# Kernel tuning notes

Measured on AMD Instinct MI355X. Metric: run time of the kernel, lower is better.

Reference implementation:

```python
import jax, jax.numpy as jnp
import numpy as np

N, IN_DIM, H, ATT_DIM, OUT_DIM = 4096, 512, 8, 64, 64
ATT_BIAS = 0.5


def setup_inputs() -> dict:
    key = jax.random.key(0)
    ks = jax.random.split(key, 12)
    s_in = 1.0 / np.sqrt(IN_DIM)
    s_o = 1.0 / np.sqrt(H * OUT_DIM)
    return {
        "Q": jax.random.normal(ks[0], (N, IN_DIM), jnp.float32),
        "K": jax.random.normal(ks[1], (N, IN_DIM), jnp.float32),
        "V": jax.random.normal(ks[2], (N, IN_DIM), jnp.float32),
        "adj": jax.random.uniform(ks[3], (N, N), jnp.float32),
        "WQ": jax.random.normal(ks[4], (IN_DIM, H * ATT_DIM), jnp.float32) * s_in,
        "bQ": jnp.zeros((H * ATT_DIM,), jnp.float32),
        "WK": jax.random.normal(ks[5], (IN_DIM, H * ATT_DIM), jnp.float32) * s_in,
        "bK": jnp.zeros((H * ATT_DIM,), jnp.float32),
        "WV": jax.random.normal(ks[6], (IN_DIM, H * OUT_DIM), jnp.float32) * s_in,
        "bV": jnp.zeros((H * OUT_DIM,), jnp.float32),
        "WO": jax.random.normal(ks[7], (H * OUT_DIM, OUT_DIM), jnp.float32) * s_o,
        "bO": jnp.zeros((OUT_DIM,), jnp.float32),
    }


def reference(Q, K, V, adj, WQ, bQ, WK, bK, WV, bV, WO, bO):
    scale = ATT_DIM ** -0.5
    q = (Q @ WQ + bQ).reshape(N, H, ATT_DIM)   # [N,H,d]
    k = (K @ WK + bK).reshape(N, H, ATT_DIM)   # [N,H,d]
    v = (V @ WV + bV).reshape(N, H, OUT_DIM)   # [N,H,e]
    # scaled QK^T per head: [H,N,N]
    scores = jnp.einsum("nhd,mhd->hnm", q * scale, k)
    # sigmoid -> bias subtract -> +0.1*adj -> softmax over keys
    scores = jax.nn.sigmoid(scores) - ATT_BIAS + 0.1 * adj[None, :, :]
    attn = jax.nn.softmax(scores, axis=2)
    # attend values (dropout p=0 => identity), concat heads, project
    out = jnp.einsum("hnm,mhe->nhe", attn, v).reshape(N, H * OUT_DIM)
    return out @ WO + bO
```

## Files before the change

kernel.cpp:

```cpp
#include <hip/hip_runtime.h>
#include <hip/hip_bf16.h>

#define N_TOK  4096
#define HD     512
#define NH     8
#define NSPLIT 4

typedef short v8s __attribute__((ext_vector_type(8)));
typedef float v4f __attribute__((ext_vector_type(4)));
typedef unsigned short u16;

#if __has_builtin(__builtin_amdgcn_exp2f)
#define USE_EXP2 1
#define ADJ_SCALE 0.14426950408889634f
#else
#define USE_EXP2 0
#define ADJ_SCALE 0.1f
#endif

__device__ __forceinline__ float bf2f(u16 x) {
  union { unsigned int u; float f; } c; c.u = ((unsigned int)x) << 16; return c.f;
}
__device__ __forceinline__ u16 f2bf(float f) {
  union { float f; unsigned int u; } c; c.f = f;
  return (u16)((c.u + 0x7fffu + ((c.u >> 16) & 1u)) >> 16);
}

__global__ void detect_k(const u16* __restrict__ q, int* __restrict__ flag) {
  int l = threadIdx.x;
  u16 e = q[2 * l];
  float x = bf2f(e);
  int ex = (e >> 7) & 0xFF;
  float ax = fabsf(x);
  bool ok = (ex != 0xFF) && (ax < 64.f) && (ax > 1e-30f);
  unsigned long long m = __ballot(ok);
  if (l == 0) *flag = (__popcll(m) >= 48) ? 0 : 1;
}

__global__ __launch_bounds__(256) void conv_qkv_k(const void* __restrict__ s0, const void* __restrict__ s1,
                                                  const void* __restrict__ s2,
                                                  u16* __restrict__ d0, u16* __restrict__ d1,
                                                  u16* __restrict__ d2, const int* __restrict__ flag) {
  int z = blockIdx.y;
  const void* s = (z == 0) ? s0 : (z == 1) ? s1 : s2;
  u16* d = (z == 0) ? d0 : (z == 1) ? d1 : d2;
  int i = blockIdx.x * 256 + threadIdx.x;
  short4 o;
  if (*flag) {
    float4 f = ((const float4*)s)[i];
    o.x = (short)f2bf(f.x); o.y = (short)f2bf(f.y);
    o.z = (short)f2bf(f.z); o.w = (short)f2bf(f.w);
  } else {
    o = ((const short4*)s)[i];
  }
  ((short4*)d)[i] = o;
}

__global__ __launch_bounds__(256) void conv_adj_k(const void* __restrict__ src, u16* __restrict__ dst,
                                                  const int* __restrict__ flag) {
  int i = blockIdx.x * 256 + threadIdx.x;
  float4 f;
  if (*flag) {
    f = ((const float4*)src)[i];
  } else {
    short4 v = ((const short4*)src)[i];
    f.x = bf2f((u16)v.x); f.y = bf2f((u16)v.y); f.z = bf2f((u16)v.z); f.w = bf2f((u16)v.w);
  }
  short4 o;
  o.x = (short)f2bf(f.x * ADJ_SCALE); o.y = (short)f2bf(f.y * ADJ_SCALE);
  o.z = (short)f2bf(f.z * ADJ_SCALE); o.w = (short)f2bf(f.w * ADJ_SCALE);
  ((short4*)dst)[i] = o;
}

__global__ void conv_bias_k(const void* sQ, const void* sK, const void* sV, const void* sO,
                            u16* dQ, u16* dK, u16* dV, u16* dO, const int* __restrict__ flag) {
  int i = blockIdx.x * 256 + threadIdx.x;
  const void* s; u16* d; int off;
  if (i < 512)       { s = sQ; d = dQ; off = i; }
  else if (i < 1024) { s = sK; d = dK; off = i - 512; }
  else if (i < 1536) { s = sV; d = dV; off = i - 1024; }
  else if (i < 1600) { s = sO; d = dO; off = i - 1536; }
  else return;
  float v = (*flag) ? ((const float*)s)[off] : bf2f(((const u16*)s)[off]);
  d[off] = f2bf(v);
}

__global__ __launch_bounds__(256) void tr_w_k(const void* W0, const void* W1, const void* W2, const void* W3,
                                              u16* t0, u16* t1, u16* t2, u16* t3,
                                              const int* __restrict__ flag) {
  int z = blockIdx.z;
  const void* in; u16* out; int C;
  if (z == 0)      { in = W0; out = t0; C = 512; }
  else if (z == 1) { in = W1; out = t1; C = 512; }
  else if (z == 2) { in = W2; out = t2; C = 512; }
  else             { in = W3; out = t3; C = 64; if (blockIdx.y) return; }
  const int R = 512;
  __shared__ __align__(16) u16 tile[64][72];
  const int r0 = blockIdx.x * 64, c0 = blockIdx.y * 64;
  const int t = threadIdx.x;
  bool f32 = (*flag) != 0;
#pragma unroll
  for (int rep = 0; rep < 2; ++rep) {
    int idx = (t + rep * 256) * 8;
    int r = idx >> 6, c = idx & 63;
    if (f32) {
      const float* sp = (const float*)in + (size_t)(r0 + r) * C + (c0 + c);
      float4 a = *(const float4*)sp, b = *(const float4*)(sp + 4);
      u16 tmp[8] = { f2bf(a.x), f2bf(a.y), f2bf(a.z), f2bf(a.w),
                     f2bf(b.x), f2bf(b.y), f2bf(b.z), f2bf(b.w) };
      *(v8s*)&tile[r][c] = *(v8s*)tmp;
    } else {
      *(v8s*)&tile[r][c] = *(const v8s*)((const u16*)in + (size_t)(r0 + r) * C + (c0 + c));
    }
  }
  __syncthreads();
#pragma unroll
  for (int rep = 0; rep < 2; ++rep) {
    int idx = (t + rep * 256) * 8;
    int oc = idx >> 6, orr = idx & 63;
    u16 tmp[8];
#pragma unroll
    for (int j = 0; j < 8; ++j) tmp[j] = tile[orr + j][oc];
    *(v8s*)(out + (size_t)(c0 + oc) * R + (r0 + orr)) = *(v8s*)tmp;
  }
}

__global__ __launch_bounds__(256) void tr_bf16(const u16* __restrict__ in, u16* __restrict__ out,
                                               int R, int C) {
  __shared__ __align__(16) u16 tile[64][72];
  const int r0 = blockIdx.x * 64, c0 = blockIdx.y * 64;
  const int t = threadIdx.x;
#pragma unroll
  for (int rep = 0; rep < 2; ++rep) {
    int idx = (t + rep * 256) * 8;
    int r = idx >> 6, c = idx & 63;
    *(v8s*)&tile[r][c] = *(const v8s*)(in + (size_t)(r0 + r) * C + (c0 + c));
  }
  __syncthreads();
#pragma unroll
  for (int rep = 0; rep < 2; ++rep) {
    int idx = (t + rep * 256) * 8;
    int oc = idx >> 6, orr = idx & 63;
    u16 tmp[8];
#pragma unroll
    for (int j = 0; j < 8; ++j) tmp[j] = tile[orr + j][oc];
    *(v8s*)(out + (size_t)(c0 + oc) * R + (r0 + orr)) = *(v8s*)tmp;
  }
}

__device__ __forceinline__ void gemm_body(const u16* __restrict__ A, const u16* __restrict__ Bt,
                                          const u16* __restrict__ bias, void* __restrict__ C,
                                          bool f32o, int NB, int K) {
  __shared__ __align__(16) u16 As[64][72];
  __shared__ __align__(16) u16 Bs[64][72];
  const int i0 = blockIdx.x * 64, j0 = blockIdx.y * 64;
  const int t = threadIdx.x, w = t >> 6, l = t & 63, quad = l >> 4, l15 = l & 15;
  v4f acc[4] = {};
  for (int k0 = 0; k0 < K; k0 += 64) {
#pragma unroll
    for (int rep = 0; rep < 2; ++rep) {
      int idx = (t + rep * 256) * 8;
      int r = idx >> 6, c = idx & 63;
      *(v8s*)&As[r][c] = *(const v8s*)(A + (size_t)(i0 + r) * K + k0 + c);
      *(v8s*)&Bs[r][c] = *(const v8s*)(Bt + (size_t)(j0 + r) * K + k0 + c);
    }
    __syncthreads();
#pragma unroll
    for (int h = 0; h < 2; ++h) {
      v8s a = *(const v8s*)&As[w * 16 + l15][h * 32 + quad * 8];
#pragma unroll
      for (int cb = 0; cb < 4; ++cb) {
        v8s b = *(const v8s*)&Bs[cb * 16 + l15][h * 32 + quad * 8];
        acc[cb] = __builtin_amdgcn_mfma_f32_16x16x32_bf16(a, b, acc[cb], 0, 0, 0);
      }
    }
    __syncthreads();
  }
#pragma unroll
  for (int cb = 0; cb < 4; ++cb) {
    int col = j0 + cb * 16 + l15;
    float bv = bf2f(bias[col]);
#pragma unroll
    for (int r = 0; r < 4; ++r) {
      int row = blockIdx.x * 64 + w * 16 + quad * 4 + r;
      float v = acc[cb][r] + bv;
      size_t idx = (size_t)row * NB + col;
      if (f32o) ((float*)C)[idx] = v;
      else      ((u16*)C)[idx] = f2bf(v);
    }
  }
}

__global__ __launch_bounds__(256) void gemm_qkv_k(const u16* __restrict__ Ac0, const u16* __restrict__ Ac1,
                                                  const u16* __restrict__ Ac2,
                                                  const u16* __restrict__ t0, const u16* __restrict__ t1,
                                                  const u16* __restrict__ t2,
                                                  const u16* __restrict__ b0, const u16* __restrict__ b1,
                                                  const u16* __restrict__ b2,
                                                  u16* __restrict__ o0, u16* __restrict__ o1,
                                                  u16* __restrict__ o2) {
  int z = blockIdx.z;
  const u16* A  = (z == 0) ? Ac0 : (z == 1) ? Ac1 : Ac2;
  const u16* Bt = (z == 0) ? t0  : (z == 1) ? t1  : t2;
  const u16* bi = (z == 0) ? b0  : (z == 1) ? b1  : b2;
  u16* C        = (z == 0) ? o0  : (z == 1) ? o1  : o2;
  gemm_body(A, Bt, bi, C, false, HD, 512);
}

__global__ __launch_bounds__(256) void gemm_bt(const u16* __restrict__ A, const u16* __restrict__ Bt,
                                               const u16* __restrict__ bias, void* __restrict__ C,
                                               const int* __restrict__ outflag, int NB, int K) {
  gemm_body(A, Bt, bias, C, (*outflag) != 0, NB, K);
}

__global__ __launch_bounds__(256) void attn_kernel(const u16* __restrict__ qb, const u16* __restrict__ kb,
                                                   const u16* __restrict__ vtb, const u16* __restrict__ adjc,
                                                   u16* __restrict__ Opart, float* __restrict__ Lpart) {
  __shared__ __align__(16) u16 Ks[64][72];
  __shared__ __align__(16) u16 Vs[64][72];
  __shared__ __align__(16) u16 Adjs[64][72];
  __shared__ __align__(16) u16 Ps[4][16][72];
  const int i0 = blockIdx.x * 64;
  const int h64 = blockIdx.y * 64;
  const int z = blockIdx.z;
  const int m_begin = z * (N_TOK / NSPLIT);
  const int m_end = m_begin + (N_TOK / NSPLIT);
  const int t = threadIdx.x, w = t >> 6, l = t & 63, quad = l >> 4, l15 = l & 15;

  v8s qf[2];
#pragma unroll
  for (int h = 0; h < 2; ++h)
    qf[h] = *(const v8s*)(qb + (size_t)(i0 + w * 16 + l15) * HD + h64 + h * 32 + quad * 8);

  v4f oacc[4] = {};
  float lsum[4] = {0.f, 0.f, 0.f, 0.f};

  for (int m0 = m_begin; m0 < m_end; m0 += 64) {
#pragma unroll
    for (int rep = 0; rep < 2; ++rep) {
      int idx = (t + rep * 256) * 8;
      int r = idx >> 6, c = idx & 63;
      *(v8s*)&Ks[r][c]   = *(const v8s*)(kb   + (size_t)(m0 + r) * HD + h64 + c);
      *(v8s*)&Vs[r][c]   = *(const v8s*)(vtb  + (size_t)(h64 + r) * N_TOK + m0 + c);
      *(v8s*)&Adjs[r][c] = *(const v8s*)(adjc + (size_t)(i0 + r) * N_TOK + m0 + c);
    }
    __syncthreads();

    v4f s[4] = {};
#pragma unroll
    for (int h = 0; h < 2; ++h) {
#pragma unroll
      for (int cb = 0; cb < 4; ++cb) {
        v8s b = *(const v8s*)&Ks[cb * 16 + l15][h * 32 + quad * 8];
        s[cb] = __builtin_amdgcn_mfma_f32_16x16x32_bf16(qf[h], b, s[cb], 0, 0, 0);
      }
    }

#pragma unroll
    for (int cb = 0; cb < 4; ++cb) {
#pragma unroll
      for (int r = 0; r < 4; ++r) {
        float sraw = s[cb][r];
        float d = bf2f(Adjs[w * 16 + quad * 4 + r][cb * 16 + l15]);
#if USE_EXP2
        float u = __builtin_amdgcn_exp2f(sraw * -0.18033688f);
        float sig = __builtin_amdgcn_rcpf(1.f + u);
        float p = __builtin_amdgcn_exp2f(fmaf(sig, 1.44269504f, d - 0.72134752f));
#else
        float u = __expf(sraw * -0.125f);
        float sig = __builtin_amdgcn_rcpf(1.f + u);
        float p = __expf(sig + (d - 0.5f));
#endif
        lsum[r] += p;
        Ps[w][quad * 4 + r][cb * 16 + l15] = f2bf(p);
      }
    }
    asm volatile("s_waitcnt lgkmcnt(0)" ::: "memory");

#pragma unroll
    for (int h = 0; h < 2; ++h) {
      v8s pa = *(const v8s*)&Ps[w][l15][h * 32 + quad * 8];
#pragma unroll
      for (int eb = 0; eb < 4; ++eb) {
        v8s vb = *(const v8s*)&Vs[eb * 16 + l15][h * 32 + quad * 8];
        oacc[eb] = __builtin_amdgcn_mfma_f32_16x16x32_bf16(pa, vb, oacc[eb], 0, 0, 0);
      }
    }
    __syncthreads();
  }

#pragma unroll
  for (int r = 0; r < 4; ++r) {
    float v = lsum[r];
    v += __shfl_xor(v, 1);
    v += __shfl_xor(v, 2);
    v += __shfl_xor(v, 4);
    v += __shfl_xor(v, 8);
    lsum[r] = v;
  }
  if (l15 == 0) {
#pragma unroll
    for (int r = 0; r < 4; ++r)
      Lpart[((size_t)z * N_TOK + i0 + w * 16 + quad * 4 + r) * NH + blockIdx.y] = lsum[r];
  }
#pragma unroll
  for (int eb = 0; eb < 4; ++eb) {
#pragma unroll
    for (int r = 0; r < 4; ++r) {
      size_t row = (size_t)z * N_TOK + i0 + w * 16 + quad * 4 + r;
      Opart[row * HD + h64 + eb * 16 + l15] = f2bf(oacc[eb][r]);
    }
  }
}

__global__ __launch_bounds__(256) void reduce_k(const u16* __restrict__ Opart, const float* __restrict__ Lpart,
                                                u16* __restrict__ ab) {
  int i = blockIdx.x * 256 + threadIdx.x;
  int row = i >> 7;
  int c4 = i & 127;
  int h = c4 >> 4;
  float lv = 0.f;
#pragma unroll
  for (int s = 0; s < NSPLIT; ++s) lv += Lpart[((size_t)s * N_TOK + row) * NH + h];
  float ax = 0.f, ay = 0.f, az = 0.f, aw = 0.f;
#pragma unroll
  for (int s = 0; s < NSPLIT; ++s) {
    short4 v = ((const short4*)Opart)[(size_t)s * (N_TOK * HD / 4) + i];
    ax += bf2f((u16)v.x); ay += bf2f((u16)v.y); az += bf2f((u16)v.z); aw += bf2f((u16)v.w);
  }
  float rl = __builtin_amdgcn_rcpf(lv);
  short4 o;
  o.x = (short)f2bf(ax * rl); o.y = (short)f2bf(ay * rl);
  o.z = (short)f2bf(az * rl); o.w = (short)f2bf(aw * rl);
  ((short4*)ab)[i] = o;
}

extern "C" void kernel_launch(void* const* d_in, const int* in_sizes, int n_in,
                              void* d_out, int out_size, void* d_ws, size_t ws_size,
                              hipStream_t stream) {
  (void)in_sizes; (void)n_in; (void)out_size; (void)ws_size;
  const void* Q   = d_in[0];
  const void* K   = d_in[1];
  const void* V   = d_in[2];
  const void* adj = d_in[3];
  const void* WQ  = d_in[4];
  const void* bQ  = d_in[5];
  const void* WK  = d_in[6];
  const void* bK  = d_in[7];
  const void* WV  = d_in[8];
  const void* bV  = d_in[9];
  const void* WO  = d_in[10];
  const void* bO  = d_in[11];

  char* p = (char*)d_ws;
  auto alloc = [&](size_t bytes) { char* r = p; p += (bytes + 255) & ~(size_t)255; return r; };
  const size_t SZ = (size_t)N_TOK * HD * 2;

  int* flag  = (int*)alloc(256);
  u16* adjc  = (u16*)alloc((size_t)N_TOK * N_TOK * 2);
  u16* Qc    = (u16*)alloc(SZ);
  u16* Kc    = (u16*)alloc(SZ);
  u16* Vc    = (u16*)alloc(SZ);
  u16* vb    = (u16*)alloc(SZ);
  u16* Opart = Qc;
  u16* qb    = (u16*)alloc(SZ);
  u16* kb    = (u16*)alloc(SZ);
  u16* vtb   = (u16*)alloc(SZ);
  u16* ab    = (u16*)alloc(SZ);
  u16* tQ    = (u16*)alloc((size_t)512 * 512 * 2);
  u16* tK    = (u16*)alloc((size_t)512 * 512 * 2);
  u16* tV    = (u16*)alloc((size_t)512 * 512 * 2);
  u16* tO    = (u16*)alloc((size_t)64 * 512 * 2);
  u16* bQc   = (u16*)alloc(512 * 2);
  u16* bKc   = (u16*)alloc(512 * 2);
  u16* bVc   = (u16*)alloc(512 * 2);
  u16* bOc   = (u16*)alloc(64 * 2);
  float* Lpart = (float*)alloc((size_t)NSPLIT * N_TOK * NH * 4);

  dim3 b256(256);
  detect_k<<<1, 64, 0, stream>>>((const u16*)Q, flag);

  conv_qkv_k<<<dim3(2048, 3), b256, 0, stream>>>(Q, K, V, Qc, Kc, Vc, flag);
  conv_adj_k<<<dim3(16384), b256, 0, stream>>>(adj, adjc, flag);
  conv_bias_k<<<dim3(7), b256, 0, stream>>>(bQ, bK, bV, bO, bQc, bKc, bVc, bOc, flag);
  tr_w_k<<<dim3(8, 8, 4), b256, 0, stream>>>(WQ, WK, WV, WO, tQ, tK, tV, tO, flag);

  gemm_qkv_k<<<dim3(64, 8, 3), b256, 0, stream>>>(Qc, Kc, Vc, tQ, tK, tV,
                                                  bQc, bKc, bVc, qb, kb, vb);

  tr_bf16<<<dim3(64, 8), b256, 0, stream>>>(vb, vtb, N_TOK, HD);

  attn_kernel<<<dim3(N_TOK / 64, NH, NSPLIT), b256, 0, stream>>>(qb, kb, vtb, adjc, Opart, Lpart);

  reduce_k<<<dim3(N_TOK * HD / 4 / 256), b256, 0, stream>>>(Opart, Lpart, ab);

  gemm_bt<<<dim3(64, 1), b256, 0, stream>>>(ab, tO, bOc, d_out, flag, 64, 512);
}
```

Before: 300.4 us.

## Precompute exp(adj), fuse input conversion into QKV GEMM, restructure attention softmax

Applies exp2 to the adjacency matrix once during conversion, so the attention inner loop multiplies by a precomputed factor instead of adding inside the exponent. The q projection scale and log2e are folded into the QKV GEMM epilogue. fp32 input conversion now happens inside the QKV GEMM loads, which removes the separate conversion kernel and its intermediate buffers, and the bias conversion is merged into the adj kernel. The attention kernel swaps MFMA operands so each lane owns one query row, loads adj straight from global memory into registers instead of staging it in LDS, writes P with packed bf16 stores, and sets a launch-bounds occupancy hint. Opart now gets its own buffer instead of aliasing Qc.

```diff
diff --git a/kernel.cpp b/kernel.cpp
--- a/kernel.cpp
+++ b/kernel.cpp
@@ -10,13 +10,9 @@
 typedef float v4f __attribute__((ext_vector_type(4)));
 typedef unsigned short u16;
 
-#if __has_builtin(__builtin_amdgcn_exp2f)
-#define USE_EXP2 1
-#define ADJ_SCALE 0.14426950408889634f
-#else
-#define USE_EXP2 0
-#define ADJ_SCALE 0.1f
-#endif
+#define QSCALE   0.18033688011112042f
+#define ADJ2     0.14426950408889634f
+#define SIG2P    1.4426950408889634f
 
 __device__ __forceinline__ float bf2f(u16 x) {
   union { unsigned int u; float f; } c; c.u = ((unsigned int)x) << 16; return c.f;
@@ -24,6 +20,18 @@
 __device__ __forceinline__ u16 f2bf(float f) {
   union { float f; unsigned int u; } c; c.f = f;
   return (u16)((c.u + 0x7fffu + ((c.u >> 16) & 1u)) >> 16);
+}
+__device__ __forceinline__ float fast_exp2(float x) {
+#if __has_builtin(__builtin_amdgcn_exp2f)
+  return __builtin_amdgcn_exp2f(x);
+#else
+  return exp2f(x);
+#endif
+}
+__device__ __forceinline__ unsigned int pk_bf16(float a, float b) {
+  union { __hip_bfloat162 h; unsigned int u; } c;
+  c.h = __float22bfloat162_rn(make_float2(a, b));
+  return c.u;
 }
 
 __global__ void detect_k(const u16* __restrict__ q, int* __restrict__ flag) {
@@ -37,52 +45,34 @@
   if (l == 0) *flag = (__popcll(m) >= 48) ? 0 : 1;
 }
 
-__global__ __launch_bounds__(256) void conv_qkv_k(const void* __restrict__ s0, const void* __restrict__ s1,
-                                                  const void* __restrict__ s2,
-                                                  u16* __restrict__ d0, u16* __restrict__ d1,
-                                                  u16* __restrict__ d2, const int* __restrict__ flag) {
-  int z = blockIdx.y;
-  const void* s = (z == 0) ? s0 : (z == 1) ? s1 : s2;
-  u16* d = (z == 0) ? d0 : (z == 1) ? d1 : d2;
-  int i = blockIdx.x * 256 + threadIdx.x;
-  short4 o;
-  if (*flag) {
-    float4 f = ((const float4*)s)[i];
-    o.x = (short)f2bf(f.x); o.y = (short)f2bf(f.y);
-    o.z = (short)f2bf(f.z); o.w = (short)f2bf(f.w);
-  } else {
-    o = ((const short4*)s)[i];
-  }
-  ((short4*)d)[i] = o;
-}
-
-__global__ __launch_bounds__(256) void conv_adj_k(const void* __restrict__ src, u16* __restrict__ dst,
-                                                  const int* __restrict__ flag) {
-  int i = blockIdx.x * 256 + threadIdx.x;
+__global__ __launch_bounds__(256) void conv_adjE_k(const void* __restrict__ adj, u16* __restrict__ adjE,
+                                                   const void* sQ, const void* sK, const void* sV, const void* sO,
+                                                   u16* dQ, u16* dK, u16* dV, u16* dO,
+                                                   const int* __restrict__ flag) {
+  int b = blockIdx.x;
+  if (b >= 16384) {
+    int i = (b - 16384) * 256 + threadIdx.x;
+    const void* s; u16* d; int off;
+    if (i < 512)       { s = sQ; d = dQ; off = i; }
+    else if (i < 1024) { s = sK; d = dK; off = i - 512; }
+    else if (i < 1536) { s = sV; d = dV; off = i - 1024; }
+    else if (i < 1600) { s = sO; d = dO; off = i - 1536; }
+    else return;
+    float v = (*flag) ? ((const float*)s)[off] : bf2f(((const u16*)s)[off]);
+    d[off] = f2bf(v);
+    return;
+  }
+  int i = b * 256 + threadIdx.x;
   float4 f;
   if (*flag) {
-    f = ((const float4*)src)[i];
+    f = ((const float4*)adj)[i];
   } else {
-    short4 v = ((const short4*)src)[i];
+    short4 v = ((const short4*)adj)[i];
     f.x = bf2f((u16)v.x); f.y = bf2f((u16)v.y); f.z = bf2f((u16)v.z); f.w = bf2f((u16)v.w);
   }
-  short4 o;
-  o.x = (short)f2bf(f.x * ADJ_SCALE); o.y = (short)f2bf(f.y * ADJ_SCALE);
-  o.z = (short)f2bf(f.z * ADJ_SCALE); o.w = (short)f2bf(f.w * ADJ_SCALE);
-  ((short4*)dst)[i] = o;
-}
-
-__global__ void conv_bias_k(const void* sQ, const void* sK, const void* sV, const void* sO,
-                            u16* dQ, u16* dK, u16* dV, u16* dO, const int* __restrict__ flag) {
-  int i = blockIdx.x * 256 + threadIdx.x;
-  const void* s; u16* d; int off;
-  if (i < 512)       { s = sQ; d = dQ; off = i; }
-  else if (i < 1024) { s = sK; d = dK; off = i - 512; }
-  else if (i < 1536) { s = sV; d = dV; off = i - 1024; }
-  else if (i < 1600) { s = sO; d = dO; off = i - 1536; }
-  else return;
-  float v = (*flag) ? ((const float*)s)[off] : bf2f(((const u16*)s)[off]);
-  d[off] = f2bf(v);
+  unsigned int d0 = pk_bf16(fast_exp2(f.x * ADJ2), fast_exp2(f.y * ADJ2));
+  unsigned int d1 = pk_bf16(fast_exp2(f.z * ADJ2), fast_exp2(f.w * ADJ2));
+  ((uint2*)adjE)[i] = make_uint2(d0, d1);
 }
 
 __global__ __launch_bounds__(256) void tr_w_k(const void* W0, const void* W1, const void* W2, const void* W3,
@@ -106,9 +96,9 @@
     if (f32) {
       const float* sp = (const float*)in + (size_t)(r0 + r) * C + (c0 + c);
       float4 a = *(const float4*)sp, b = *(const float4*)(sp + 4);
-      u16 tmp[8] = { f2bf(a.x), f2bf(a.y), f2bf(a.z), f2bf(a.w),
-                     f2bf(b.x), f2bf(b.y), f2bf(b.z), f2bf(b.w) };
-      *(v8s*)&tile[r][c] = *(v8s*)tmp;
+      uint4 q = make_uint4(pk_bf16(a.x, a.y), pk_bf16(a.z, a.w),
+                           pk_bf16(b.x, b.y), pk_bf16(b.z, b.w));
+      *(uint4*)&tile[r][c] = q;
     } else {
       *(v8s*)&tile[r][c] = *(const v8s*)((const u16*)in + (size_t)(r0 + r) * C + (c0 + c));
     }
@@ -148,9 +138,67 @@
   }
 }
 
-__device__ __forceinline__ void gemm_body(const u16* __restrict__ A, const u16* __restrict__ Bt,
-                                          const u16* __restrict__ bias, void* __restrict__ C,
-                                          bool f32o, int NB, int K) {
+__global__ __launch_bounds__(256) void gemm_qkv_k(const void* A0, const void* A1, const void* A2,
+                                                  const u16* __restrict__ t0, const u16* __restrict__ t1,
+                                                  const u16* __restrict__ t2,
+                                                  const u16* b0, const u16* b1, const u16* b2,
+                                                  u16* o0, u16* o1, u16* o2,
+                                                  const int* __restrict__ flag) {
+  __shared__ __align__(16) u16 As[64][72];
+  __shared__ __align__(16) u16 Bs[64][72];
+  int z = blockIdx.z;
+  const void* Araw = (z == 0) ? A0 : (z == 1) ? A1 : A2;
+  const u16* Bt    = (z == 0) ? t0 : (z == 1) ? t1 : t2;
+  const u16* bias  = (z == 0) ? b0 : (z == 1) ? b1 : b2;
+  u16* C           = (z == 0) ? o0 : (z == 1) ? o1 : o2;
+  const float oscale = (z == 0) ? QSCALE : 1.0f;
+  const bool f32 = (*flag) != 0;
+  const int i0 = blockIdx.x * 64, j0 = blockIdx.y * 64;
+  const int t = threadIdx.x, w = t >> 6, l = t & 63, quad = l >> 4, l15 = l & 15;
+  v4f acc[4] = {};
+  for (int k0 = 0; k0 < 512; k0 += 64) {
+#pragma unroll
+    for (int rep = 0; rep < 2; ++rep) {
+      int idx = (t + rep * 256) * 8;
+      int r = idx >> 6, c = idx & 63;
+      if (f32) {
+        const float* sp = (const float*)Araw + (size_t)(i0 + r) * 512 + k0 + c;
+        float4 fa = *(const float4*)sp, fb = *(const float4*)(sp + 4);
+        uint4 q = make_uint4(pk_bf16(fa.x, fa.y), pk_bf16(fa.z, fa.w),
+                             pk_bf16(fb.x, fb.y), pk_bf16(fb.z, fb.w));
+        *(uint4*)&As[r][c] = q;
+      } else {
+        *(v8s*)&As[r][c] = *(const v8s*)((const u16*)Araw + (size_t)(i0 + r) * 512 + k0 + c);
+      }
+      *(v8s*)&Bs[r][c] = *(const v8s*)(Bt + (size_t)(j0 + r) * 512 + k0 + c);
+    }
+    __syncthreads();
+#pragma unroll
+    for (int h = 0; h < 2; ++h) {
+      v8s a = *(const v8s*)&As[w * 16 + l15][h * 32 + quad * 8];
+#pragma unroll
+      for (int cb = 0; cb < 4; ++cb) {
+        v8s b = *(const v8s*)&Bs[cb * 16 + l15][h * 32 + quad * 8];
+        acc[cb] = __builtin_amdgcn_mfma_f32_16x16x32_bf16(a, b, acc[cb], 0, 0, 0);
+      }
+    }
+    __syncthreads();
+  }
+#pragma unroll
+  for (int cb = 0; cb < 4; ++cb) {
+    int col = j0 + cb * 16 + l15;
+    float bv = bf2f(bias[col]);
+#pragma unroll
+    for (int r = 0; r < 4; ++r) {
+      int row = i0 + w * 16 + quad * 4 + r;
+      C[(size_t)row * HD + col] = f2bf((acc[cb][r] + bv) * oscale);
+    }
+  }
+}
+
+__global__ __launch_bounds__(256) void gemm_bt(const u16* __restrict__ A, const u16* __restrict__ Bt,
+                                               const u16* __restrict__ bias, void* __restrict__ C,
+                                               const int* __restrict__ outflag, int NB, int K) {
   __shared__ __align__(16) u16 As[64][72];
   __shared__ __align__(16) u16 Bs[64][72];
   const int i0 = blockIdx.x * 64, j0 = blockIdx.y * 64;
@@ -176,13 +224,14 @@
     }
     __syncthreads();
   }
+  bool f32o = (*outflag) != 0;
 #pragma unroll
   for (int cb = 0; cb < 4; ++cb) {
     int col = j0 + cb * 16 + l15;
     float bv = bf2f(bias[col]);
 #pragma unroll
     for (int r = 0; r < 4; ++r) {
-      int row = blockIdx.x * 64 + w * 16 + quad * 4 + r;
+      int row = i0 + w * 16 + quad * 4 + r;
       float v = acc[cb][r] + bv;
       size_t idx = (size_t)row * NB + col;
       if (f32o) ((float*)C)[idx] = v;
@@ -191,58 +240,38 @@
   }
 }
 
-__global__ __launch_bounds__(256) void gemm_qkv_k(const u16* __restrict__ Ac0, const u16* __restrict__ Ac1,
-                                                  const u16* __restrict__ Ac2,
-                                                  const u16* __restrict__ t0, const u16* __restrict__ t1,
-                                                  const u16* __restrict__ t2,
-                                                  const u16* __restrict__ b0, const u16* __restrict__ b1,
-                                                  const u16* __restrict__ b2,
-                                                  u16* __restrict__ o0, u16* __restrict__ o1,
-                                                  u16* __restrict__ o2) {
-  int z = blockIdx.z;
-  const u16* A  = (z == 0) ? Ac0 : (z == 1) ? Ac1 : Ac2;
-  const u16* Bt = (z == 0) ? t0  : (z == 1) ? t1  : t2;
-  const u16* bi = (z == 0) ? b0  : (z == 1) ? b1  : b2;
-  u16* C        = (z == 0) ? o0  : (z == 1) ? o1  : o2;
-  gemm_body(A, Bt, bi, C, false, HD, 512);
-}
-
-__global__ __launch_bounds__(256) void gemm_bt(const u16* __restrict__ A, const u16* __restrict__ Bt,
-                                               const u16* __restrict__ bias, void* __restrict__ C,
-                                               const int* __restrict__ outflag, int NB, int K) {
-  gemm_body(A, Bt, bias, C, (*outflag) != 0, NB, K);
-}
-
-__global__ __launch_bounds__(256) void attn_kernel(const u16* __restrict__ qb, const u16* __restrict__ kb,
-                                                   const u16* __restrict__ vtb, const u16* __restrict__ adjc,
-                                                   u16* __restrict__ Opart, float* __restrict__ Lpart) {
+__global__ __launch_bounds__(256, 5) void attn_kernel(const u16* __restrict__ qb, const u16* __restrict__ kb,
+                                                      const u16* __restrict__ vtb, const u16* __restrict__ adjE,
+                                                      u16* __restrict__ Opart, float* __restrict__ Lpart) {
   __shared__ __align__(16) u16 Ks[64][72];
   __shared__ __align__(16) u16 Vs[64][72];
-  __shared__ __align__(16) u16 Adjs[64][72];
   __shared__ __align__(16) u16 Ps[4][16][72];
-  const int i0 = blockIdx.x * 64;
-  const int h64 = blockIdx.y * 64;
-  const int z = blockIdx.z;
+  const int i0 = blockIdx.x * 64, h64 = blockIdx.y * 64, z = blockIdx.z;
+  const int t = threadIdx.x, w = t >> 6, l = t & 63, quad = l >> 4, l15 = l & 15;
+  const int iRow = i0 + w * 16 + l15;
+
+  v8s qf[2];
+#pragma unroll
+  for (int h = 0; h < 2; ++h)
+    qf[h] = *(const v8s*)(qb + (size_t)iRow * HD + h64 + h * 32 + quad * 8);
+
+  const u16* adjRow = adjE + (size_t)iRow * N_TOK;
+  v4f oacc[4] = {};
+  float lsum = 0.f;
+
   const int m_begin = z * (N_TOK / NSPLIT);
-  const int m_end = m_begin + (N_TOK / NSPLIT);
-  const int t = threadIdx.x, w = t >> 6, l = t & 63, quad = l >> 4, l15 = l & 15;
-
-  v8s qf[2];
-#pragma unroll
-  for (int h = 0; h < 2; ++h)
-    qf[h] = *(const v8s*)(qb + (size_t)(i0 + w * 16 + l15) * HD + h64 + h * 32 + quad * 8);
-
-  v4f oacc[4] = {};
-  float lsum[4] = {0.f, 0.f, 0.f, 0.f};
-
-  for (int m0 = m_begin; m0 < m_end; m0 += 64) {
+  for (int m0 = m_begin; m0 < m_begin + N_TOK / NSPLIT; m0 += 64) {
+    uint2 av[4];
+#pragma unroll
+    for (int cb = 0; cb < 4; ++cb)
+      av[cb] = *(const uint2*)(adjRow + m0 + cb * 16 + quad * 4);
+
 #pragma unroll
     for (int rep = 0; rep < 2; ++rep) {
       int idx = (t + rep * 256) * 8;
       int r = idx >> 6, c = idx & 63;
-      *(v8s*)&Ks[r][c]   = *(const v8s*)(kb   + (size_t)(m0 + r) * HD + h64 + c);
-      *(v8s*)&Vs[r][c]   = *(const v8s*)(vtb  + (size_t)(h64 + r) * N_TOK + m0 + c);
-      *(v8s*)&Adjs[r][c] = *(const v8s*)(adjc + (size_t)(i0 + r) * N_TOK + m0 + c);
+      *(v8s*)&Ks[r][c] = *(const v8s*)(kb  + (size_t)(m0 + r) * HD + h64 + c);
+      *(v8s*)&Vs[r][c] = *(const v8s*)(vtb + (size_t)(h64 + r) * N_TOK + m0 + c);
     }
     __syncthreads();
 
@@ -251,29 +280,25 @@
     for (int h = 0; h < 2; ++h) {
 #pragma unroll
       for (int cb = 0; cb < 4; ++cb) {
-        v8s b = *(const v8s*)&Ks[cb * 16 + l15][h * 32 + quad * 8];
-        s[cb] = __builtin_amdgcn_mfma_f32_16x16x32_bf16(qf[h], b, s[cb], 0, 0, 0);
+        v8s kf = *(const v8s*)&Ks[cb * 16 + l15][h * 32 + quad * 8];
+        s[cb] = __builtin_amdgcn_mfma_f32_16x16x32_bf16(kf, qf[h], s[cb], 0, 0, 0);
       }
     }
 
 #pragma unroll
     for (int cb = 0; cb < 4; ++cb) {
-#pragma unroll
-      for (int r = 0; r < 4; ++r) {
-        float sraw = s[cb][r];
-        float d = bf2f(Adjs[w * 16 + quad * 4 + r][cb * 16 + l15]);
-#if USE_EXP2
-        float u = __builtin_amdgcn_exp2f(sraw * -0.18033688f);
-        float sig = __builtin_amdgcn_rcpf(1.f + u);
-        float p = __builtin_amdgcn_exp2f(fmaf(sig, 1.44269504f, d - 0.72134752f));
-#else
-        float u = __expf(sraw * -0.125f);
-        float sig = __builtin_amdgcn_rcpf(1.f + u);
-        float p = __expf(sig + (d - 0.5f));
-#endif
-        lsum[r] += p;
-        Ps[w][quad * 4 + r][cb * 16 + l15] = f2bf(p);
-      }
+      union { unsigned int u; float f; } e0, e1, e2, e3;
+      e0.u = av[cb].x << 16; e1.u = av[cb].x & 0xFFFF0000u;
+      e2.u = av[cb].y << 16; e3.u = av[cb].y & 0xFFFF0000u;
+      float p0, p1, p2, p3;
+      {
+        float u0 = fast_exp2(-s[cb][0]); p0 = fast_exp2(__builtin_amdgcn_rcpf(1.f + u0) * SIG2P) * e0.f;
+        float u1 = fast_exp2(-s[cb][1]); p1 = fast_exp2(__builtin_amdgcn_rcpf(1.f + u1) * SIG2P) * e1.f;
+        float u2 = fast_exp2(-s[cb][2]); p2 = fast_exp2(__builtin_amdgcn_rcpf(1.f + u2) * SIG2P) * e2.f;
+        float u3 = fast_exp2(-s[cb][3]); p3 = fast_exp2(__builtin_amdgcn_rcpf(1.f + u3) * SIG2P) * e3.f;
+      }
+      lsum += (p0 + p1) + (p2 + p3);
+      *(uint2*)&Ps[w][l15][cb * 16 + quad * 4] = make_uint2(pk_bf16(p0, p1), pk_bf16(p2, p3));
     }
     asm volatile("s_waitcnt lgkmcnt(0)" ::: "memory");
 
@@ -282,27 +307,17 @@
       v8s pa = *(const v8s*)&Ps[w][l15][h * 32 + quad * 8];
 #pragma unroll
       for (int eb = 0; eb < 4; ++eb) {
-        v8s vb = *(const v8s*)&Vs[eb * 16 + l15][h * 32 + quad * 8];
-        oacc[eb] = __builtin_amdgcn_mfma_f32_16x16x32_bf16(pa, vb, oacc[eb], 0, 0, 0);
-      }
-    }
-    __syncthreads();
-  }
-
-#pragma unroll
-  for (int r = 0; r < 4; ++r) {
-    float v = lsum[r];
-    v += __shfl_xor(v, 1);
-    v += __shfl_xor(v, 2);
-    v += __shfl_xor(v, 4);
-    v += __shfl_xor(v, 8);
-    lsum[r] = v;
-  }
-  if (l15 == 0) {
-#pragma unroll
-    for (int r = 0; r < 4; ++r)
-      Lpart[((size_t)z * N_TOK + i0 + w * 16 + quad * 4 + r) * NH + blockIdx.y] = lsum[r];
-  }
+        v8s vf = *(const v8s*)&Vs[eb * 16 + l15][h * 32 + quad * 8];
+        oacc[eb] = __builtin_amdgcn_mfma_f32_16x16x32_bf16(pa, vf, oacc[eb], 0, 0, 0);
+      }
+    }
+    __syncthreads();
+  }
+
+  lsum += __shfl_xor(lsum, 16);
+  lsum += __shfl_xor(lsum, 32);
+  if (l < 16)
+    Lpart[((size_t)z * N_TOK + i0 + w * 16 + l) * NH + blockIdx.y] = lsum;
 #pragma unroll
   for (int eb = 0; eb < 4; ++eb) {
 #pragma unroll
@@ -329,10 +344,7 @@
     ax += bf2f((u16)v.x); ay += bf2f((u16)v.y); az += bf2f((u16)v.z); aw += bf2f((u16)v.w);
   }
   float rl = __builtin_amdgcn_rcpf(lv);
-  short4 o;
-  o.x = (short)f2bf(ax * rl); o.y = (short)f2bf(ay * rl);
-  o.z = (short)f2bf(az * rl); o.w = (short)f2bf(aw * rl);
-  ((short4*)ab)[i] = o;
+  ((uint2*)ab)[i] = make_uint2(pk_bf16(ax * rl, ay * rl), pk_bf16(az * rl, aw * rl));
 }
 
 extern "C" void kernel_launch(void* const* d_in, const int* in_sizes, int n_in,
@@ -356,41 +368,37 @@
   auto alloc = [&](size_t bytes) { char* r = p; p += (bytes + 255) & ~(size_t)255; return r; };
   const size_t SZ = (size_t)N_TOK * HD * 2;
 
-  int* flag  = (int*)alloc(256);
-  u16* adjc  = (u16*)alloc((size_t)N_TOK * N_TOK * 2);
-  u16* Qc    = (u16*)alloc(SZ);
-  u16* Kc    = (u16*)alloc(SZ);
-  u16* Vc    = (u16*)alloc(SZ);
-  u16* vb    = (u16*)alloc(SZ);
-  u16* Opart = Qc;
-  u16* qb    = (u16*)alloc(SZ);
-  u16* kb    = (u16*)alloc(SZ);
-  u16* vtb   = (u16*)alloc(SZ);
-  u16* ab    = (u16*)alloc(SZ);
-  u16* tQ    = (u16*)alloc((size_t)512 * 512 * 2);
-  u16* tK    = (u16*)alloc((size_t)512 * 512 * 2);
-  u16* tV    = (u16*)alloc((size_t)512 * 512 * 2);
-  u16* tO    = (u16*)alloc((size_t)64 * 512 * 2);
-  u16* bQc   = (u16*)alloc(512 * 2);
-  u16* bKc   = (u16*)alloc(512 * 2);
-  u16* bVc   = (u16*)alloc(512 * 2);
-  u16* bOc   = (u16*)alloc(64 * 2);
+  int* flag    = (int*)alloc(256);
+  u16* adjE    = (u16*)alloc((size_t)N_TOK * N_TOK * 2);
+  u16* qb      = (u16*)alloc(SZ);
+  u16* kb      = (u16*)alloc(SZ);
+  u16* vb      = (u16*)alloc(SZ);
+  u16* vtb     = (u16*)alloc(SZ);
+  u16* ab      = (u16*)alloc(SZ);
+  u16* Opart   = (u16*)alloc((size_t)NSPLIT * SZ);
   float* Lpart = (float*)alloc((size_t)NSPLIT * N_TOK * NH * 4);
+  u16* tQ      = (u16*)alloc((size_t)512 * 512 * 2);
+  u16* tK      = (u16*)alloc((size_t)512 * 512 * 2);
+  u16* tV      = (u16*)alloc((size_t)512 * 512 * 2);
+  u16* tO      = (u16*)alloc((size_t)64 * 512 * 2);
+  u16* bQc     = (u16*)alloc(512 * 2);
+  u16* bKc     = (u16*)alloc(512 * 2);
+  u16* bVc     = (u16*)alloc(512 * 2);
+  u16* bOc     = (u16*)alloc(64 * 2);
 
   dim3 b256(256);
   detect_k<<<1, 64, 0, stream>>>((const u16*)Q, flag);
 
-  conv_qkv_k<<<dim3(2048, 3), b256, 0, stream>>>(Q, K, V, Qc, Kc, Vc, flag);
-  conv_adj_k<<<dim3(16384), b256, 0, stream>>>(adj, adjc, flag);
-  conv_bias_k<<<dim3(7), b256, 0, stream>>>(bQ, bK, bV, bO, bQc, bKc, bVc, bOc, flag);
+  conv_adjE_k<<<dim3(16384 + 7), b256, 0, stream>>>(adj, adjE, bQ, bK, bV, bO,
+                                                    bQc, bKc, bVc, bOc, flag);
   tr_w_k<<<dim3(8, 8, 4), b256, 0, stream>>>(WQ, WK, WV, WO, tQ, tK, tV, tO, flag);
 
-  gemm_qkv_k<<<dim3(64, 8, 3), b256, 0, stream>>>(Qc, Kc, Vc, tQ, tK, tV,
-                                                  bQc, bKc, bVc, qb, kb, vb);
+  gemm_qkv_k<<<dim3(64, 8, 3), b256, 0, stream>>>(Q, K, V, tQ, tK, tV,
+                                                  bQc, bKc, bVc, qb, kb, vb, flag);
 
   tr_bf16<<<dim3(64, 8), b256, 0, stream>>>(vb, vtb, N_TOK, HD);
 
-  attn_kernel<<<dim3(N_TOK / 64, NH, NSPLIT), b256, 0, stream>>>(qb, kb, vtb, adjc, Opart, Lpart);
+  attn_kernel<<<dim3(N_TOK / 64, NH, NSPLIT), b256, 0, stream>>>(qb, kb, vtb, adjE, Opart, Lpart);
 
   reduce_k<<<dim3(N_TOK * HD / 4 / 256), b256, 0, stream>>>(Opart, Lpart, ab);
 
```

Result: faster. 274.2 us (-8.7%).
